# Kernel optimization log

Hardware: AMD Instinct MI355X
Metric: run time of the kernel (lower is better)

The kernel has to match this reference:

```python
import jax, jax.numpy as jnp
import numpy as np

B, T, V, H, OUT = 1024, 128, 89, 256, 1


def setup_inputs() -> dict:
    key = jax.random.key(0)
    ks = jax.random.split(key, 16)
    x = jax.random.normal(ks[0], (B, T, V), dtype=jnp.float32)
    mask = (jax.random.uniform(ks[1], (B, T, V)) < 0.7).astype(jnp.float32)
    deltas = jax.random.uniform(ks[2], (B, T, V), dtype=jnp.float32)
    meanset = jax.random.normal(ks[3], (V,), dtype=jnp.float32)

    def uni(k, shape, fan):
        s = 1.0 / np.sqrt(fan)
        return jax.random.uniform(k, shape, jnp.float32, -s, s)

    # Decay h: Linear(V -> H); Decay x: diag Linear(V -> V)
    W_h = uni(ks[4], (H, V), V)
    b_h = uni(ks[5], (H,), V)
    W_x = uni(ks[6], (V, V), V)
    b_x = uni(ks[7], (V,), V)
    # GRUCell(2V -> H), torch layout: W_ih [3H, 2V], W_hh [3H, H]
    W_ih = uni(ks[8], (3 * H, 2 * V), 2 * V)
    b_ih = uni(ks[9], (3 * H,), 2 * V)
    W_hh = uni(ks[10], (3 * H, H), H)
    b_hh = uni(ks[11], (3 * H,), H)
    # classification head
    W_cls = uni(ks[12], (OUT, H), H)
    b_cls = uni(ks[13], (OUT,), H)
    return {"x": x, "mask": mask, "deltas": deltas, "meanset": meanset,
            "W_h": W_h, "b_h": b_h, "W_x": W_x, "b_x": b_x,
            "W_ih": W_ih, "b_ih": b_ih, "W_hh": W_hh, "b_hh": b_hh,
            "W_cls": W_cls, "b_cls": b_cls}


def reference(x, mask, deltas, meanset, W_h, b_h, W_x, b_x,
              W_ih, b_ih, W_hh, b_hh, W_cls, b_cls):
    Bn, Tn, Vn = x.shape
    Hn = W_h.shape[0]
    # diag Decay: W * eye(V) -> only the diagonal of W_x contributes
    w_x_diag = jnp.diagonal(W_x)

    def step(carry, inp):
        h, last, loss = carry
        x_t, m_t, d_t = inp  # each [B, V]
        gamma_h = jnp.exp(-jax.nn.relu(d_t @ W_h.T + b_h))          # [B, H]
        gamma_x = jnp.exp(-jax.nn.relu(d_t * w_x_diag + b_x))       # [B, V]
        # forward-fill (pandas ffill includes current observation)
        last = jnp.where(m_t > 0, x_t, last)
        h = h * gamma_h
        x_u = gamma_x * last + (1.0 - gamma_x) * meanset
        loss = loss + jnp.sum(jnp.abs(x_t - x_u) * m_t) / (jnp.sum(m_t) + 1e-5)
        x_h = m_t * x_t + (1.0 - m_t) * x_u
        inp_cat = jnp.concatenate([x_h, m_t], axis=1)               # [B, 2V]
        gi = inp_cat @ W_ih.T + b_ih
        gh = h @ W_hh.T + b_hh
        i_r, i_z, i_n = jnp.split(gi, 3, axis=1)
        h_r, h_z, h_n = jnp.split(gh, 3, axis=1)
        r = jax.nn.sigmoid(i_r + h_r)
        z = jax.nn.sigmoid(i_z + h_z)
        n = jnp.tanh(i_n + r * h_n)
        h = (1.0 - z) * n + z * h
        return (h, last, loss), x_h

    init = (jnp.zeros((Bn, Hn), x.dtype), jnp.zeros((Bn, Vn), x.dtype),
            jnp.zeros((), x.dtype))
    xs = (jnp.swapaxes(x, 0, 1), jnp.swapaxes(mask, 0, 1), jnp.swapaxes(deltas, 0, 1))
    (h, _, x_loss), ximp = jax.lax.scan(step, init, xs)
    x_imp = jnp.swapaxes(ximp, 0, 1)                                # [B, T, V]
    # dropout is identity at eval time
    y_out = h @ W_cls.T + b_cls
    y_score = jax.nn.sigmoid(y_out)
    return x_imp, x_loss, y_out, y_score
```

## Files before the change

### kernel.cpp

```cpp
#include <hip/hip_runtime.h>

#define B_  1024
#define T_  128
#define V_  89
#define H_  256
#define NB2 256

typedef __attribute__((ext_vector_type(8))) short bf16x8;
typedef __attribute__((ext_vector_type(4))) float f32x4;
typedef __attribute__((ext_vector_type(4))) unsigned short u16x4;
typedef __attribute__((ext_vector_type(8))) int i32x8;
typedef __attribute__((ext_vector_type(4))) int i32x4;

__device__ __forceinline__ short f2bs(float f){
    unsigned u = __float_as_uint(f);
    unsigned r = (u + 0x7FFFu + ((u>>16)&1u)) >> 16;
    return (short)r;
}
__device__ __forceinline__ float s2f(unsigned short s){
    return __uint_as_float(((unsigned)s) << 16);
}
__device__ __forceinline__ float sig_(float x){ return 1.f/(1.f+__expf(-x)); }
__device__ __forceinline__ float tanh_(float x){ return 2.f/(1.f+__expf(-2.f*x)) - 1.f; }

__global__ __launch_bounds__(256) void k_cvt_fp8(
    const float* __restrict__ src, unsigned char* __restrict__ dst, int n)
{
    int i = blockIdx.x*256 + threadIdx.x;
    if (i*4 >= n) return;
    float f0 = src[i*4+0], f1 = src[i*4+1], f2 = src[i*4+2], f3 = src[i*4+3];
    int w = __builtin_amdgcn_cvt_pk_fp8_f32(f0, f1, 0, false);
    w     = __builtin_amdgcn_cvt_pk_fp8_f32(f2, f3, w, true);
    ((int*)dst)[i] = w;
}

__global__ __launch_bounds__(256) void k_prep_wih8(
    const float* __restrict__ W_ih, const float* __restrict__ b_ih,
    unsigned char* __restrict__ dst)
{
    int i = blockIdx.x*256 + threadIdx.x;
    if (i >= 18432) return;
    int l15 = i & 15, t = i >> 4;
    int g8 = t & 3; t >>= 2;
    int kt = t % 6; t /= 6;
    int g = t % 3, WV = t / 3;
    int n = g*256 + WV*16 + l15;
    float f[8];
    #pragma unroll
    for (int j = 0; j < 8; ++j) {
        int k = kt*32 + g8*8 + j;
        f[j] = (k < 178) ? W_ih[(size_t)n*178 + k] : (k == 178 ? b_ih[n] : 0.f);
    }
    int w0 = __builtin_amdgcn_cvt_pk_fp8_f32(f[0], f[1], 0, false);
    w0     = __builtin_amdgcn_cvt_pk_fp8_f32(f[2], f[3], w0, true);
    int w1 = __builtin_amdgcn_cvt_pk_fp8_f32(f[4], f[5], 0, false);
    w1     = __builtin_amdgcn_cvt_pk_fp8_f32(f[6], f[7], w1, true);
    ((int*)dst)[i*2]   = w0;
    ((int*)dst)[i*2+1] = w1;
}

__global__ __launch_bounds__(256) void k_prep_whp(
    const float* __restrict__ W_h, const float* __restrict__ b_h,
    short* __restrict__ dst)
{
    int i = blockIdx.x*256 + threadIdx.x;
    if (i >= 256*96) return;
    int n = i / 96, k = i - n*96;
    float v = (k < V_) ? W_h[(size_t)n*V_ + k] : (k == V_ ? b_h[n] : 0.f);
    dst[i] = f2bs(v);
}

__global__ __launch_bounds__(512) void k_prep(
    const float* __restrict__ x, const float* __restrict__ mask,
    const float* __restrict__ deltas, const float* __restrict__ meanset,
    const float* __restrict__ W_x, const float* __restrict__ b_x,
    const unsigned char* __restrict__ wihT, const short* __restrict__ whp,
    float* __restrict__ ximp, float* __restrict__ lastst,
    float* __restrict__ numpart, float* __restrict__ denpart,
    unsigned short* __restrict__ gi4, int t0, int TC, int first)
{
    __shared__ unsigned char xl[16*200] __attribute__((aligned(16)));
    __shared__ short dl2[16*104] __attribute__((aligned(16)));
    __shared__ float lossn[4][360], lossd[4][360];
    int tid = threadIdx.x, lane = tid & 63, wv = tid >> 6;
    int l15 = lane & 15, g8 = lane >> 4;
    int blk = blockIdx.x;

    for (int i = tid; i < 16*22; i += 512) {
        int r = i/22, k = 178 + (i - r*22);
        xl[r*200 + k] = (k == 178) ? 0x38 : 0;
    }
    for (int i = tid; i < 16*15; i += 512) {
        int r = i/15, k = 89 + (i - r*15);
        dl2[r*104 + k] = (k == 89) ? (short)0x3F80 : (short)0;
    }
    bool own = tid < 4*V_;
    int r_o = tid / V_, v_o = tid - r_o*V_, b_o = blk*4 + r_o;
    float wxd = 0.f, bx = 0.f, mnv = 0.f, lastv = 0.f;
    if (own) {
        wxd = W_x[v_o*V_ + v_o]; bx = b_x[v_o]; mnv = meanset[v_o];
        lastv = first ? 0.f : lastst[(size_t)b_o*V_ + v_o];
    }
    const long* wT = (const long*)wihT;

    int nph = TC >> 2;
    for (int p = 0; p < nph; ++p) {
        int tg = t0 + p*4;
        __syncthreads();
        if (own) {
            const float* xb = x      + ((size_t)b_o*T_ + tg)*V_ + v_o;
            const float* mb = mask   + ((size_t)b_o*T_ + tg)*V_ + v_o;
            const float* db = deltas + ((size_t)b_o*T_ + tg)*V_ + v_o;
            float xv[4], mv[4], dv[4];
            #pragma unroll
            for (int lt = 0; lt < 4; ++lt) {
                xv[lt] = xb[lt*V_]; mv[lt] = mb[lt*V_]; dv[lt] = db[lt*V_];
            }
            #pragma unroll
            for (int lt = 0; lt < 4; ++lt) {
                float xt = xv[lt], m = mv[lt], d = dv[lt];
                float gx = __expf(-fmaxf(fmaf(d, wxd, bx), 0.f));
                lastv = (m > 0.f) ? xt : lastv;
                float xu = gx*lastv + (1.f-gx)*mnv;
                float xh = m*xt + (1.f-m)*xu;
                ximp[((size_t)b_o*T_ + tg + lt)*V_ + v_o] = xh;
                int mr = r_o*4 + lt;
                int pk = __builtin_amdgcn_cvt_pk_fp8_f32(xh, m, 0, false);
                xl[mr*200 + v_o]      = (unsigned char)(pk & 0xFF);
                xl[mr*200 + V_ + v_o] = (unsigned char)((pk >> 8) & 0xFF);
                dl2[mr*104 + v_o]     = f2bs(d);
                lossn[lt][tid] = fabsf(xt - xu)*m;
                lossd[lt][tid] = m;
            }
        }
        __syncthreads();
        if (tid < 64) {
            int lt = tid >> 4, part = tid & 15;
            float n = 0.f, ds = 0.f;
            for (int j = part; j < 4*V_; j += 16) { n += lossn[lt][j]; ds += lossd[lt][j]; }
            n += __shfl_xor(n, 1); ds += __shfl_xor(ds, 1);
            n += __shfl_xor(n, 2); ds += __shfl_xor(ds, 2);
            n += __shfl_xor(n, 4); ds += __shfl_xor(ds, 4);
            n += __shfl_xor(n, 8); ds += __shfl_xor(ds, 8);
            if (part == 0) {
                numpart[(size_t)(tg+lt)*NB2 + blk] = n;
                denpart[(size_t)(tg+lt)*NB2 + blk] = ds;
            }
        }
        #pragma unroll
        for (int s = 0; s < 2; ++s) {
            int cset = wv + s*8;
            size_t iw = (size_t)cset*1152 + g8*16 + l15;
            f32x4 ar = {0.f,0.f,0.f,0.f}, az = ar, an = ar, ga = ar;
            #pragma unroll
            for (int kt = 0; kt < 6; ++kt) {
                long a = *(const long*)&xl[l15*200 + kt*32 + g8*8];
                ar = __builtin_amdgcn_mfma_f32_16x16x32_fp8_fp8(a, wT[iw +       kt*64], ar, 0,0,0);
                az = __builtin_amdgcn_mfma_f32_16x16x32_fp8_fp8(a, wT[iw + 384 + kt*64], az, 0,0,0);
                an = __builtin_amdgcn_mfma_f32_16x16x32_fp8_fp8(a, wT[iw + 768 + kt*64], an, 0,0,0);
            }
            int cg = cset*16 + l15;
            #pragma unroll
            for (int kt = 0; kt < 3; ++kt) {
                bf16x8 da = *(const bf16x8*)&dl2[l15*104 + kt*32 + g8*8];
                bf16x8 gw = *(const bf16x8*)(whp + (size_t)cg*96 + kt*32 + g8*8);
                ga = __builtin_amdgcn_mfma_f32_16x16x32_bf16(da, gw, ga, 0,0,0);
            }
            #pragma unroll
            for (int rr = 0; rr < 4; ++rr) {
                int ltc = p*4 + rr;
                u16x4 v;
                v[0] = (unsigned short)f2bs(ar[rr]);
                v[1] = (unsigned short)f2bs(az[rr]);
                v[2] = (unsigned short)f2bs(an[rr]);
                v[3] = (unsigned short)f2bs(__expf(-fmaxf(ga[rr], 0.f)));
                ((u16x4*)gi4)[(((size_t)ltc*256 + blk)*4 + g8)*256 + cg] = v;
            }
        }
    }
    if (own) lastst[(size_t)b_o*V_ + v_o] = lastv;
}

__global__ __launch_bounds__(512) void k_recur(
    const unsigned short* __restrict__ gi4, const unsigned char* __restrict__ whh8,
    const float* __restrict__ b_hh, const float* __restrict__ W_cls,
    const float* __restrict__ b_cls,
    float* __restrict__ hstate, float* __restrict__ yout, float* __restrict__ yscore,
    int TC, int first, int last)
{
    __shared__ unsigned char whL[256*256];
    __shared__ unsigned char hlds[2][4*272] __attribute__((aligned(16)));
    __shared__ float yred[4][8];

    int tid = threadIdx.x, lane = tid & 63, wv = tid >> 6;
    int l15 = lane & 15, g8 = lane >> 4;
    int blk = blockIdx.x;
    int c0 = wv*16 + l15, c1 = c0 + 128;

    for (int it = 0; it < 16; ++it) {
        int idx = it*512 + tid;
        int row = idx >> 5, j = idx & 31;
        long v = *(const long*)(whh8 + (size_t)row*256 + j*8);
        *(long*)&whL[row*256 + ((j*8) ^ ((row & 15) << 4))] = v;
    }
    i32x8 wz[2][2], wn[2][2];
    #pragma unroll
    for (int s = 0; s < 2; ++s) {
        int cs16 = (wv + s*8)*16 + l15;
        #pragma unroll
        for (int k2 = 0; k2 < 2; ++k2) {
            wz[s][k2] = *(const i32x8*)(whh8 + (size_t)(256 + cs16)*256 + k2*128 + g8*32);
            wn[s][k2] = *(const i32x8*)(whh8 + (size_t)(512 + cs16)*256 + k2*128 + g8*32);
        }
    }
    float bhr[2], bhz[2], bhn[2];
    #pragma unroll
    for (int s = 0; s < 2; ++s) {
        int cs16 = (wv + s*8)*16 + l15;
        bhr[s] = b_hh[cs16]; bhz[s] = b_hh[256 + cs16]; bhn[s] = b_hh[512 + cs16];
    }

    float h0 = first ? 0.f : hstate[(size_t)(blk*4 + g8)*H_ + c0];
    float h1 = first ? 0.f : hstate[(size_t)(blk*4 + g8)*H_ + c1];

    __syncthreads();

    const u16x4* gp = (const u16x4*)gi4;
#define GIDX(LT,C) ((((size_t)(LT)*256 + blk)*4 + g8)*256 + (C))
    u16x4 gv0 = gp[GIDX(0, c0)], gv1 = gp[GIDX(0, c1)];

    for (int lt = 0; lt < TC; ++lt) {
        int cb = lt & 1;
        float hd0 = h0 * s2f(gv0[3]);
        float hd1 = h1 * s2f(gv1[3]);
        int pk = __builtin_amdgcn_cvt_pk_fp8_f32(hd0, hd1, 0, false);
        hlds[cb][g8*272 + c0] = (unsigned char)(pk & 0xFF);
        hlds[cb][g8*272 + c1] = (unsigned char)((pk >> 8) & 0xFF);
        __syncthreads();
        i32x8 A[2];
        #pragma unroll
        for (int k2 = 0; k2 < 2; ++k2) {
            const unsigned char* ap = &hlds[cb][(l15 >> 2)*272 + k2*128 + g8*32];
            i32x4 lo = *(const i32x4*)(ap);
            i32x4 hi = *(const i32x4*)(ap + 16);
            i32x8 a; a[0]=lo[0]; a[1]=lo[1]; a[2]=lo[2]; a[3]=lo[3];
                     a[4]=hi[0]; a[5]=hi[1]; a[6]=hi[2]; a[7]=hi[3];
            A[k2] = a;
        }
        u16x4 ngv0 = gv0, ngv1 = gv1;
        if (lt + 1 < TC) { ngv0 = gp[GIDX(lt+1, c0)]; ngv1 = gp[GIDX(lt+1, c1)]; }
        int sw = l15 << 4;
        #pragma unroll
        for (int s = 0; s < 2; ++s) {
            const unsigned char* wb = &whL[(size_t)((wv + s*8)*16 + l15)*256];
            f32x4 sr = {bhr[s],bhr[s],bhr[s],bhr[s]};
            f32x4 sz = {bhz[s],bhz[s],bhz[s],bhz[s]};
            f32x4 sn = {bhn[s],bhn[s],bhn[s],bhn[s]};
            #pragma unroll
            for (int k2 = 0; k2 < 2; ++k2) {
                int ob = k2*128 + g8*32;
                i32x4 blo = *(const i32x4*)(wb + ((ob     ) ^ sw));
                i32x4 bhi = *(const i32x4*)(wb + ((ob + 16) ^ sw));
                i32x8 b; b[0]=blo[0]; b[1]=blo[1]; b[2]=blo[2]; b[3]=blo[3];
                         b[4]=bhi[0]; b[5]=bhi[1]; b[6]=bhi[2]; b[7]=bhi[3];
                sr = __builtin_amdgcn_mfma_scale_f32_16x16x128_f8f6f4(A[k2], b,         sr, 0,0, 0,0x7F7F7F7F, 0,0x7F7F7F7F);
                sz = __builtin_amdgcn_mfma_scale_f32_16x16x128_f8f6f4(A[k2], wz[s][k2], sz, 0,0, 0,0x7F7F7F7F, 0,0x7F7F7F7F);
                sn = __builtin_amdgcn_mfma_scale_f32_16x16x128_f8f6f4(A[k2], wn[s][k2], sn, 0,0, 0,0x7F7F7F7F, 0,0x7F7F7F7F);
            }
            if (s == 0) {
                float rg = sig_(s2f(gv0[0]) + sr[0]);
                float zg = sig_(s2f(gv0[1]) + sz[0]);
                float ng = tanh_(s2f(gv0[2]) + rg*sn[0]);
                h0 = (1.f - zg)*ng + zg*hd0;
            } else {
                float rg = sig_(s2f(gv1[0]) + sr[0]);
                float zg = sig_(s2f(gv1[1]) + sz[0]);
                float ng = tanh_(s2f(gv1[2]) + rg*sn[0]);
                h1 = (1.f - zg)*ng + zg*hd1;
            }
        }
        gv0 = ngv0; gv1 = ngv1;
    }
#undef GIDX

    hstate[(size_t)(blk*4 + g8)*H_ + c0] = h0;
    hstate[(size_t)(blk*4 + g8)*H_ + c1] = h1;

    if (last) {
        float pr = h0 * W_cls[c0] + h1 * W_cls[c1];
        pr += __shfl_xor(pr, 1);
        pr += __shfl_xor(pr, 2);
        pr += __shfl_xor(pr, 4);
        pr += __shfl_xor(pr, 8);
        if (l15 == 0) yred[g8][wv] = pr;
        __syncthreads();
        if (tid < 4) {
            float sacc = b_cls[0];
            #pragma unroll
            for (int ww = 0; ww < 8; ++ww) sacc += yred[tid][ww];
            yout[blk*4 + tid]   = sacc;
            yscore[blk*4 + tid] = 1.f/(1.f+__expf(-sacc));
        }
    }
}

__global__ __launch_bounds__(256) void k_loss_t(
    const float* __restrict__ numpart, const float* __restrict__ denpart,
    float* __restrict__ tpart)
{
    int t = blockIdx.x, tid = threadIdx.x;
    float n = numpart[(size_t)t*NB2 + tid];
    float d = denpart[(size_t)t*NB2 + tid];
    for (int off = 32; off; off >>= 1) { n += __shfl_down(n, off); d += __shfl_down(d, off); }
    __shared__ float sn[4], sd[4];
    int lane = tid & 63, wid = tid >> 6;
    if (lane == 0) { sn[wid] = n; sd[wid] = d; }
    __syncthreads();
    if (tid == 0) {
        float nn = sn[0]+sn[1]+sn[2]+sn[3], dd = sd[0]+sd[1]+sd[2]+sd[3];
        tpart[t] = nn / (dd + 1e-5f);
    }
}

__global__ __launch_bounds__(128) void k_loss_final(
    const float* __restrict__ tpart, float* __restrict__ out_loss)
{
    int tid = threadIdx.x;
    float s = tpart[tid];
    for (int off = 32; off; off >>= 1) s += __shfl_down(s, off);
    __shared__ float sp[2];
    if ((tid&63)==0) sp[tid>>6] = s;
    __syncthreads();
    if (tid==0) out_loss[0] = sp[0] + sp[1];
}

static inline size_t al256(size_t x){ return (x + 255) & ~(size_t)255; }

extern "C" void kernel_launch(void* const* d_in, const int* in_sizes, int n_in,
                              void* d_out, int out_size, void* d_ws, size_t ws_size,
                              hipStream_t stream)
{
    const float* x      = (const float*)d_in[0];
    const float* mask   = (const float*)d_in[1];
    const float* deltas = (const float*)d_in[2];
    const float* meanset= (const float*)d_in[3];
    const float* W_h    = (const float*)d_in[4];
    const float* b_h    = (const float*)d_in[5];
    const float* W_x    = (const float*)d_in[6];
    const float* b_x    = (const float*)d_in[7];
    const float* W_ih   = (const float*)d_in[8];
    const float* b_ih   = (const float*)d_in[9];
    const float* W_hh   = (const float*)d_in[10];
    const float* b_hh   = (const float*)d_in[11];
    const float* W_cls  = (const float*)d_in[12];
    const float* b_cls  = (const float*)d_in[13];

    float* out    = (float*)d_out;
    float* ximp   = out;
    float* xloss  = out + (size_t)B_*T_*V_;
    float* yout   = xloss + 1;
    float* yscore = yout + B_;

    size_t off = 0;
    size_t off_whh8 = off; off = al256(off + (size_t)768*256);
    size_t off_wihT = off; off = al256(off + (size_t)768*192);
    size_t off_whp  = off; off = al256(off + (size_t)256*96*2);
    size_t off_last = off; off = al256(off + (size_t)B_*V_*4);
    size_t off_h    = off; off = al256(off + (size_t)B_*H_*4);
    size_t off_np   = off; off = al256(off + (size_t)T_*NB2*4);
    size_t off_dp   = off; off = al256(off + (size_t)T_*NB2*4);
    size_t off_tp   = off; off = al256(off + (size_t)T_*4);
    size_t off_gi4  = off;

    int tcShift = -1;
    for (int s = 7; s >= 2; --s) {
        size_t gib = (size_t)(1 << s) * 256 * 4 * 256 * 8;
        if (off_gi4 + gib <= ws_size) { tcShift = s; break; }
    }
    if (tcShift < 0) return;
    int TC = 1 << tcShift;
    int NC = T_ / TC;

    char* ws = (char*)d_ws;
    unsigned char* whh8 = (unsigned char*)(ws + off_whh8);
    unsigned char* wihT = (unsigned char*)(ws + off_wihT);
    short* whp    = (short*)(ws + off_whp);
    float* lastst = (float*)(ws + off_last);
    float* hstate = (float*)(ws + off_h);
    float* numpart= (float*)(ws + off_np);
    float* denpart= (float*)(ws + off_dp);
    float* tpart  = (float*)(ws + off_tp);
    unsigned short* gi4 = (unsigned short*)(ws + off_gi4);

    hipLaunchKernelGGL(k_cvt_fp8, dim3((768*256/4+255)/256), dim3(256), 0, stream, W_hh, whh8, 768*256);
    hipLaunchKernelGGL(k_prep_wih8, dim3((18432+255)/256), dim3(256), 0, stream, W_ih, b_ih, wihT);
    hipLaunchKernelGGL(k_prep_whp, dim3((256*96+255)/256), dim3(256), 0, stream, W_h, b_h, whp);

    for (int ci = 0; ci < NC; ++ci) {
        int t0 = ci * TC;
        hipLaunchKernelGGL(k_prep, dim3(256), dim3(512), 0, stream,
                           x, mask, deltas, meanset, W_x, b_x, wihT, whp,
                           ximp, lastst, numpart, denpart, gi4, t0, TC, ci==0);
        hipLaunchKernelGGL(k_recur, dim3(256), dim3(512), 0, stream,
                           gi4, whh8, b_hh, W_cls, b_cls,
                           hstate, yout, yscore, TC, ci==0, ci==NC-1);
    }
    hipLaunchKernelGGL(k_loss_t, dim3(T_), dim3(256), 0, stream, numpart, denpart, tpart);
    hipLaunchKernelGGL(k_loss_final, dim3(1), dim3(128), 0, stream, tpart, xloss);
}
```

Before: 269.0 us.

## Split imputation into its own kernel, parallelize gate GEMM over time, widen recurrence blocks

Imputation and the forward-fill scan move into a dedicated kernel with one thread per (batch, variable). It writes an fp8 packed x/mask buffer and per-wave loss partials, so the serial time loop no longer sits inside the gate kernel. The gate projection becomes a separate kernel with a 2D grid over time groups, so all timesteps in a chunk are computed in parallel. The recurrence kernel uses 1024 threads with one hidden column per thread instead of two, and prefetches gates two steps ahead. The cost is an extra global round trip through the fp8 buffer, a serial 128-step loop in the imputation kernel, and higher register pressure in the recurrence.

```diff
diff --git a/kernel.cpp b/kernel.cpp
--- a/kernel.cpp
+++ b/kernel.cpp
@@ -5,6 +5,8 @@
 #define V_  89
 #define H_  256
 #define NB2 256
+#define NBLK1 356
+#define NW1   (NBLK1*4)
 
 typedef __attribute__((ext_vector_type(8))) short bf16x8;
 typedef __attribute__((ext_vector_type(4))) float f32x4;
@@ -70,118 +72,109 @@
     dst[i] = f2bs(v);
 }
 
-__global__ __launch_bounds__(512) void k_prep(
+__global__ __launch_bounds__(256) void k_impute(
     const float* __restrict__ x, const float* __restrict__ mask,
     const float* __restrict__ deltas, const float* __restrict__ meanset,
     const float* __restrict__ W_x, const float* __restrict__ b_x,
+    float* __restrict__ ximp, unsigned char* __restrict__ xm8,
+    float* __restrict__ num_part, float* __restrict__ den_part)
+{
+    int tid = threadIdx.x;
+    int i = blockIdx.x*256 + tid;
+    int b = i / V_, v = i - b*V_;
+    float wxd = W_x[v*V_ + v];
+    float bx  = b_x[v];
+    float mv  = meanset[v];
+    const float* xp = x      + (size_t)b*T_*V_ + v;
+    const float* mp = mask   + (size_t)b*T_*V_ + v;
+    const float* dp = deltas + (size_t)b*T_*V_ + v;
+    float*       op = ximp   + (size_t)b*T_*V_ + v;
+    unsigned char* qp = xm8  + ((size_t)b*T_*V_ + v)*2;
+    float last = 0.f;
+    int lane = tid & 63, wid = tid >> 6;
+    int gw = blockIdx.x*4 + wid;
+    for (int t = 0; t < T_; ++t) {
+        float xt = xp[t*V_], m = mp[t*V_], d = dp[t*V_];
+        float g = __expf(-fmaxf(fmaf(d, wxd, bx), 0.f));
+        last = (m > 0.f) ? xt : last;
+        float xu = g*last + (1.f-g)*mv;
+        float xh = m*xt + (1.f-m)*xu;
+        op[t*V_] = xh;
+        int pk = __builtin_amdgcn_cvt_pk_fp8_f32(xh, m, 0, false);
+        *(unsigned short*)(qp + (size_t)t*V_*2) = (unsigned short)(pk & 0xFFFF);
+        float nv = fabsf(xt - xu)*m;
+        float dv = m;
+        for (int off = 32; off; off >>= 1) {
+            nv += __shfl_down(nv, off);
+            dv += __shfl_down(dv, off);
+        }
+        if (lane == 0) { num_part[t*NW1 + gw] = nv; den_part[t*NW1 + gw] = dv; }
+    }
+}
+
+__global__ __launch_bounds__(512) void k_gates(
+    const unsigned char* __restrict__ xm8, const float* __restrict__ deltas,
     const unsigned char* __restrict__ wihT, const short* __restrict__ whp,
-    float* __restrict__ ximp, float* __restrict__ lastst,
-    float* __restrict__ numpart, float* __restrict__ denpart,
-    unsigned short* __restrict__ gi4, int t0, int TC, int first)
+    unsigned short* __restrict__ gi4, int t0)
 {
     __shared__ unsigned char xl[16*200] __attribute__((aligned(16)));
     __shared__ short dl2[16*104] __attribute__((aligned(16)));
-    __shared__ float lossn[4][360], lossd[4][360];
     int tid = threadIdx.x, lane = tid & 63, wv = tid >> 6;
     int l15 = lane & 15, g8 = lane >> 4;
-    int blk = blockIdx.x;
-
-    for (int i = tid; i < 16*22; i += 512) {
-        int r = i/22, k = 178 + (i - r*22);
+    int bg = blockIdx.x, ph = blockIdx.y;
+    int tg = t0 + ph*4;
+
+    for (int i = tid; i < 16*14; i += 512) {
+        int r = i/14, k = 178 + (i - r*14);
         xl[r*200 + k] = (k == 178) ? 0x38 : 0;
     }
     for (int i = tid; i < 16*15; i += 512) {
         int r = i/15, k = 89 + (i - r*15);
         dl2[r*104 + k] = (k == 89) ? (short)0x3F80 : (short)0;
     }
-    bool own = tid < 4*V_;
-    int r_o = tid / V_, v_o = tid - r_o*V_, b_o = blk*4 + r_o;
-    float wxd = 0.f, bx = 0.f, mnv = 0.f, lastv = 0.f;
-    if (own) {
-        wxd = W_x[v_o*V_ + v_o]; bx = b_x[v_o]; mnv = meanset[v_o];
-        lastv = first ? 0.f : lastst[(size_t)b_o*V_ + v_o];
-    }
+    for (int i = tid; i < 16*V_; i += 512) {
+        int r = i / V_, v = i - r*V_;
+        int b = bg*4 + (r >> 2), t = tg + (r & 3);
+        unsigned short pk = *(const unsigned short*)(xm8 + ((size_t)(b*T_ + t)*V_ + v)*2);
+        xl[r*200 + v]      = (unsigned char)(pk & 0xFF);
+        xl[r*200 + V_ + v] = (unsigned char)(pk >> 8);
+        dl2[r*104 + v]     = f2bs(deltas[((size_t)b*T_ + t)*V_ + v]);
+    }
+    __syncthreads();
     const long* wT = (const long*)wihT;
-
-    int nph = TC >> 2;
-    for (int p = 0; p < nph; ++p) {
-        int tg = t0 + p*4;
-        __syncthreads();
-        if (own) {
-            const float* xb = x      + ((size_t)b_o*T_ + tg)*V_ + v_o;
-            const float* mb = mask   + ((size_t)b_o*T_ + tg)*V_ + v_o;
-            const float* db = deltas + ((size_t)b_o*T_ + tg)*V_ + v_o;
-            float xv[4], mv[4], dv[4];
-            #pragma unroll
-            for (int lt = 0; lt < 4; ++lt) {
-                xv[lt] = xb[lt*V_]; mv[lt] = mb[lt*V_]; dv[lt] = db[lt*V_];
-            }
-            #pragma unroll
-            for (int lt = 0; lt < 4; ++lt) {
-                float xt = xv[lt], m = mv[lt], d = dv[lt];
-                float gx = __expf(-fmaxf(fmaf(d, wxd, bx), 0.f));
-                lastv = (m > 0.f) ? xt : lastv;
-                float xu = gx*lastv + (1.f-gx)*mnv;
-                float xh = m*xt + (1.f-m)*xu;
-                ximp[((size_t)b_o*T_ + tg + lt)*V_ + v_o] = xh;
-                int mr = r_o*4 + lt;
-                int pk = __builtin_amdgcn_cvt_pk_fp8_f32(xh, m, 0, false);
-                xl[mr*200 + v_o]      = (unsigned char)(pk & 0xFF);
-                xl[mr*200 + V_ + v_o] = (unsigned char)((pk >> 8) & 0xFF);
-                dl2[mr*104 + v_o]     = f2bs(d);
-                lossn[lt][tid] = fabsf(xt - xu)*m;
-                lossd[lt][tid] = m;
-            }
-        }
-        __syncthreads();
-        if (tid < 64) {
-            int lt = tid >> 4, part = tid & 15;
-            float n = 0.f, ds = 0.f;
-            for (int j = part; j < 4*V_; j += 16) { n += lossn[lt][j]; ds += lossd[lt][j]; }
-            n += __shfl_xor(n, 1); ds += __shfl_xor(ds, 1);
-            n += __shfl_xor(n, 2); ds += __shfl_xor(ds, 2);
-            n += __shfl_xor(n, 4); ds += __shfl_xor(ds, 4);
-            n += __shfl_xor(n, 8); ds += __shfl_xor(ds, 8);
-            if (part == 0) {
-                numpart[(size_t)(tg+lt)*NB2 + blk] = n;
-                denpart[(size_t)(tg+lt)*NB2 + blk] = ds;
-            }
-        }
-        #pragma unroll
-        for (int s = 0; s < 2; ++s) {
-            int cset = wv + s*8;
-            size_t iw = (size_t)cset*1152 + g8*16 + l15;
-            f32x4 ar = {0.f,0.f,0.f,0.f}, az = ar, an = ar, ga = ar;
-            #pragma unroll
-            for (int kt = 0; kt < 6; ++kt) {
-                long a = *(const long*)&xl[l15*200 + kt*32 + g8*8];
-                ar = __builtin_amdgcn_mfma_f32_16x16x32_fp8_fp8(a, wT[iw +       kt*64], ar, 0,0,0);
-                az = __builtin_amdgcn_mfma_f32_16x16x32_fp8_fp8(a, wT[iw + 384 + kt*64], az, 0,0,0);
-                an = __builtin_amdgcn_mfma_f32_16x16x32_fp8_fp8(a, wT[iw + 768 + kt*64], an, 0,0,0);
-            }
-            int cg = cset*16 + l15;
-            #pragma unroll
-            for (int kt = 0; kt < 3; ++kt) {
-                bf16x8 da = *(const bf16x8*)&dl2[l15*104 + kt*32 + g8*8];
-                bf16x8 gw = *(const bf16x8*)(whp + (size_t)cg*96 + kt*32 + g8*8);
-                ga = __builtin_amdgcn_mfma_f32_16x16x32_bf16(da, gw, ga, 0,0,0);
-            }
-            #pragma unroll
-            for (int rr = 0; rr < 4; ++rr) {
-                int ltc = p*4 + rr;
-                u16x4 v;
-                v[0] = (unsigned short)f2bs(ar[rr]);
-                v[1] = (unsigned short)f2bs(az[rr]);
-                v[2] = (unsigned short)f2bs(an[rr]);
-                v[3] = (unsigned short)f2bs(__expf(-fmaxf(ga[rr], 0.f)));
-                ((u16x4*)gi4)[(((size_t)ltc*256 + blk)*4 + g8)*256 + cg] = v;
-            }
-        }
-    }
-    if (own) lastst[(size_t)b_o*V_ + v_o] = lastv;
-}
-
-__global__ __launch_bounds__(512) void k_recur(
+    #pragma unroll
+    for (int s = 0; s < 2; ++s) {
+        int cset = wv + s*8;
+        size_t iw = (size_t)cset*1152 + g8*16 + l15;
+        f32x4 ar = {0.f,0.f,0.f,0.f}, az = ar, an = ar, ga = ar;
+        #pragma unroll
+        for (int kt = 0; kt < 6; ++kt) {
+            long a = *(const long*)&xl[l15*200 + kt*32 + g8*8];
+            ar = __builtin_amdgcn_mfma_f32_16x16x32_fp8_fp8(a, wT[iw +       kt*64], ar, 0,0,0);
+            az = __builtin_amdgcn_mfma_f32_16x16x32_fp8_fp8(a, wT[iw + 384 + kt*64], az, 0,0,0);
+            an = __builtin_amdgcn_mfma_f32_16x16x32_fp8_fp8(a, wT[iw + 768 + kt*64], an, 0,0,0);
+        }
+        int cg = cset*16 + l15;
+        #pragma unroll
+        for (int kt = 0; kt < 3; ++kt) {
+            bf16x8 da = *(const bf16x8*)&dl2[l15*104 + kt*32 + g8*8];
+            bf16x8 gw = *(const bf16x8*)(whp + (size_t)cg*96 + kt*32 + g8*8);
+            ga = __builtin_amdgcn_mfma_f32_16x16x32_bf16(da, gw, ga, 0,0,0);
+        }
+        #pragma unroll
+        for (int rr = 0; rr < 4; ++rr) {
+            int ltc = ph*4 + rr;
+            u16x4 v;
+            v[0] = (unsigned short)f2bs(ar[rr]);
+            v[1] = (unsigned short)f2bs(az[rr]);
+            v[2] = (unsigned short)f2bs(an[rr]);
+            v[3] = (unsigned short)f2bs(__expf(-fmaxf(ga[rr], 0.f)));
+            ((u16x4*)gi4)[(((size_t)ltc*256 + bg)*4 + g8)*256 + cg] = v;
+        }
+    }
+}
+
+__global__ __launch_bounds__(1024) void k_recur(
     const unsigned short* __restrict__ gi4, const unsigned char* __restrict__ whh8,
     const float* __restrict__ b_hh, const float* __restrict__ W_cls,
     const float* __restrict__ b_cls,
@@ -190,53 +183,53 @@
 {
     __shared__ unsigned char whL[256*256];
     __shared__ unsigned char hlds[2][4*272] __attribute__((aligned(16)));
-    __shared__ float yred[4][8];
-
-    int tid = threadIdx.x, lane = tid & 63, wv = tid >> 6;
+    __shared__ float yred[4][16];
+
+    int tid = threadIdx.x, lane = tid & 63, wv16 = tid >> 6;
     int l15 = lane & 15, g8 = lane >> 4;
     int blk = blockIdx.x;
-    int c0 = wv*16 + l15, c1 = c0 + 128;
-
-    for (int it = 0; it < 16; ++it) {
-        int idx = it*512 + tid;
+    int c = wv16*16 + l15;
+
+    #pragma unroll
+    for (int it = 0; it < 8; ++it) {
+        int idx = it*1024 + tid;
         int row = idx >> 5, j = idx & 31;
         long v = *(const long*)(whh8 + (size_t)row*256 + j*8);
         *(long*)&whL[row*256 + ((j*8) ^ ((row & 15) << 4))] = v;
     }
-    i32x8 wz[2][2], wn[2][2];
-    #pragma unroll
-    for (int s = 0; s < 2; ++s) {
-        int cs16 = (wv + s*8)*16 + l15;
-        #pragma unroll
-        for (int k2 = 0; k2 < 2; ++k2) {
-            wz[s][k2] = *(const i32x8*)(whh8 + (size_t)(256 + cs16)*256 + k2*128 + g8*32);
-            wn[s][k2] = *(const i32x8*)(whh8 + (size_t)(512 + cs16)*256 + k2*128 + g8*32);
-        }
-    }
-    float bhr[2], bhz[2], bhn[2];
-    #pragma unroll
-    for (int s = 0; s < 2; ++s) {
-        int cs16 = (wv + s*8)*16 + l15;
-        bhr[s] = b_hh[cs16]; bhz[s] = b_hh[256 + cs16]; bhn[s] = b_hh[512 + cs16];
-    }
-
-    float h0 = first ? 0.f : hstate[(size_t)(blk*4 + g8)*H_ + c0];
-    float h1 = first ? 0.f : hstate[(size_t)(blk*4 + g8)*H_ + c1];
-
+    i32x8 wz[2], wn[2];
+    #pragma unroll
+    for (int k2 = 0; k2 < 2; ++k2) {
+        wz[k2] = *(const i32x8*)(whh8 + (size_t)(256 + c)*256 + k2*128 + g8*32);
+        wn[k2] = *(const i32x8*)(whh8 + (size_t)(512 + c)*256 + k2*128 + g8*32);
+    }
+    #pragma unroll
+    for (int k2 = 0; k2 < 2; ++k2) {
+        #pragma unroll
+        for (int j = 0; j < 8; ++j) {
+            asm volatile("" : "+v"(wz[k2][j]));
+            asm volatile("" : "+v"(wn[k2][j]));
+        }
+    }
+    float bhr = b_hh[c], bhz = b_hh[256 + c], bhn = b_hh[512 + c];
+    float h = first ? 0.f : hstate[(size_t)(blk*4 + g8)*H_ + c];
     __syncthreads();
 
     const u16x4* gp = (const u16x4*)gi4;
-#define GIDX(LT,C) ((((size_t)(LT)*256 + blk)*4 + g8)*256 + (C))
-    u16x4 gv0 = gp[GIDX(0, c0)], gv1 = gp[GIDX(0, c1)];
+#define GIDX(LT) ((((size_t)(LT)*256 + blk)*4 + g8)*256 + c)
+    u16x4 gv0 = gp[GIDX(0)];
+    u16x4 gv1 = (TC > 1) ? gp[GIDX(1)] : gv0;
+    int sw = l15 << 4;
+    const unsigned char* wb = &whL[(size_t)c*256];
 
     for (int lt = 0; lt < TC; ++lt) {
         int cb = lt & 1;
-        float hd0 = h0 * s2f(gv0[3]);
-        float hd1 = h1 * s2f(gv1[3]);
-        int pk = __builtin_amdgcn_cvt_pk_fp8_f32(hd0, hd1, 0, false);
-        hlds[cb][g8*272 + c0] = (unsigned char)(pk & 0xFF);
-        hlds[cb][g8*272 + c1] = (unsigned char)((pk >> 8) & 0xFF);
+        float hd = h * s2f(gv0[3]);
+        int pk = __builtin_amdgcn_cvt_pk_fp8_f32(hd, hd, 0, false);
+        hlds[cb][g8*272 + c] = (unsigned char)(pk & 0xFF);
         __syncthreads();
+        u16x4 gv2 = gv1;
+        if (lt + 2 < TC) gv2 = gp[GIDX(lt + 2)];
         i32x8 A[2];
         #pragma unroll
         for (int k2 = 0; k2 < 2; ++k2) {
@@ -247,57 +240,42 @@
                      a[4]=hi[0]; a[5]=hi[1]; a[6]=hi[2]; a[7]=hi[3];
             A[k2] = a;
         }
-        u16x4 ngv0 = gv0, ngv1 = gv1;
-        if (lt + 1 < TC) { ngv0 = gp[GIDX(lt+1, c0)]; ngv1 = gp[GIDX(lt+1, c1)]; }
-        int sw = l15 << 4;
-        #pragma unroll
-        for (int s = 0; s < 2; ++s) {
-            const unsigned char* wb = &whL[(size_t)((wv + s*8)*16 + l15)*256];
-            f32x4 sr = {bhr[s],bhr[s],bhr[s],bhr[s]};
-            f32x4 sz = {bhz[s],bhz[s],bhz[s],bhz[s]};
-            f32x4 sn = {bhn[s],bhn[s],bhn[s],bhn[s]};
-            #pragma unroll
-            for (int k2 = 0; k2 < 2; ++k2) {
-                int ob = k2*128 + g8*32;
-                i32x4 blo = *(const i32x4*)(wb + ((ob     ) ^ sw));
-                i32x4 bhi = *(const i32x4*)(wb + ((ob + 16) ^ sw));
-                i32x8 b; b[0]=blo[0]; b[1]=blo[1]; b[2]=blo[2]; b[3]=blo[3];
-                         b[4]=bhi[0]; b[5]=bhi[1]; b[6]=bhi[2]; b[7]=bhi[3];
-                sr = __builtin_amdgcn_mfma_scale_f32_16x16x128_f8f6f4(A[k2], b,         sr, 0,0, 0,0x7F7F7F7F, 0,0x7F7F7F7F);
-                sz = __builtin_amdgcn_mfma_scale_f32_16x16x128_f8f6f4(A[k2], wz[s][k2], sz, 0,0, 0,0x7F7F7F7F, 0,0x7F7F7F7F);
-                sn = __builtin_amdgcn_mfma_scale_f32_16x16x128_f8f6f4(A[k2], wn[s][k2], sn, 0,0, 0,0x7F7F7F7F, 0,0x7F7F7F7F);
-            }
-            if (s == 0) {
-                float rg = sig_(s2f(gv0[0]) + sr[0]);
-                float zg = sig_(s2f(gv0[1]) + sz[0]);
-                float ng = tanh_(s2f(gv0[2]) + rg*sn[0]);
-                h0 = (1.f - zg)*ng + zg*hd0;
-            } else {
-                float rg = sig_(s2f(gv1[0]) + sr[0]);
-                float zg = sig_(s2f(gv1[1]) + sz[0]);
-                float ng = tanh_(s2f(gv1[2]) + rg*sn[0]);
-                h1 = (1.f - zg)*ng + zg*hd1;
-            }
-        }
-        gv0 = ngv0; gv1 = ngv1;
+        f32x4 sr = {bhr,bhr,bhr,bhr};
+        f32x4 sz = {bhz,bhz,bhz,bhz};
+        f32x4 sn = {bhn,bhn,bhn,bhn};
+        #pragma unroll
+        for (int k2 = 0; k2 < 2; ++k2) {
+            int ob = k2*128 + g8*32;
+            i32x4 blo = *(const i32x4*)(wb + ((ob     ) ^ sw));
+            i32x4 bhi = *(const i32x4*)(wb + ((ob + 16) ^ sw));
+            i32x8 b; b[0]=blo[0]; b[1]=blo[1]; b[2]=blo[2]; b[3]=blo[3];
+                     b[4]=bhi[0]; b[5]=bhi[1]; b[6]=bhi[2]; b[7]=bhi[3];
+            sr = __builtin_amdgcn_mfma_scale_f32_16x16x128_f8f6f4(A[k2], b,      sr, 0,0, 0,0x7F7F7F7F, 0,0x7F7F7F7F);
+            sz = __builtin_amdgcn_mfma_scale_f32_16x16x128_f8f6f4(A[k2], wz[k2], sz, 0,0, 0,0x7F7F7F7F, 0,0x7F7F7F7F);
+            sn = __builtin_amdgcn_mfma_scale_f32_16x16x128_f8f6f4(A[k2], wn[k2], sn, 0,0, 0,0x7F7F7F7F, 0,0x7F7F7F7F);
+        }
+        float rg = sig_(s2f(gv0[0]) + sr[0]);
+        float zg = sig_(s2f(gv0[1]) + sz[0]);
+        float ng = tanh_(s2f(gv0[2]) + rg*sn[0]);
+        h = (1.f - zg)*ng + zg*hd;
+        gv0 = gv1; gv1 = gv2;
     }
 #undef GIDX
 
-    hstate[(size_t)(blk*4 + g8)*H_ + c0] = h0;
-    hstate[(size_t)(blk*4 + g8)*H_ + c1] = h1;
+    hstate[(size_t)(blk*4 + g8)*H_ + c] = h;
 
     if (last) {
-        float pr = h0 * W_cls[c0] + h1 * W_cls[c1];
+        float pr = h * W_cls[c];
         pr += __shfl_xor(pr, 1);
         pr += __shfl_xor(pr, 2);
         pr += __shfl_xor(pr, 4);
         pr += __shfl_xor(pr, 8);
-        if (l15 == 0) yred[g8][wv] = pr;
+        if (l15 == 0) yred[g8][wv16] = pr;
         __syncthreads();
         if (tid < 4) {
             float sacc = b_cls[0];
             #pragma unroll
-            for (int ww = 0; ww < 8; ++ww) sacc += yred[tid][ww];
+            for (int ww = 0; ww < 16; ++ww) sacc += yred[tid][ww];
             yout[blk*4 + tid]   = sacc;
             yscore[blk*4 + tid] = 1.f/(1.f+__expf(-sacc));
         }
@@ -305,20 +283,20 @@
 }
 
 __global__ __launch_bounds__(256) void k_loss_t(
-    const float* __restrict__ numpart, const float* __restrict__ denpart,
+    const float* __restrict__ num_part, const float* __restrict__ den_part,
     float* __restrict__ tpart)
 {
     int t = blockIdx.x, tid = threadIdx.x;
-    float n = numpart[(size_t)t*NB2 + tid];
-    float d = denpart[(size_t)t*NB2 + tid];
-    for (int off = 32; off; off >>= 1) { n += __shfl_down(n, off); d += __shfl_down(d, off); }
+    float num = 0.f, den = 0.f;
+    for (int j = tid; j < NW1; j += 256) { num += num_part[t*NW1+j]; den += den_part[t*NW1+j]; }
+    for (int off = 32; off; off >>= 1) { num += __shfl_down(num, off); den += __shfl_down(den, off); }
     __shared__ float sn[4], sd[4];
     int lane = tid & 63, wid = tid >> 6;
-    if (lane == 0) { sn[wid] = n; sd[wid] = d; }
+    if (lane == 0) { sn[wid] = num; sd[wid] = den; }
     __syncthreads();
     if (tid == 0) {
-        float nn = sn[0]+sn[1]+sn[2]+sn[3], dd = sd[0]+sd[1]+sd[2]+sd[3];
-        tpart[t] = nn / (dd + 1e-5f);
+        float n = sn[0]+sn[1]+sn[2]+sn[3], d = sd[0]+sd[1]+sd[2]+sd[3];
+        tpart[t] = n / (d + 1e-5f);
     }
 }
 
@@ -365,10 +343,10 @@
     size_t off_whh8 = off; off = al256(off + (size_t)768*256);
     size_t off_wihT = off; off = al256(off + (size_t)768*192);
     size_t off_whp  = off; off = al256(off + (size_t)256*96*2);
-    size_t off_last = off; off = al256(off + (size_t)B_*V_*4);
+    size_t off_xm8  = off; off = al256(off + (size_t)B_*T_*V_*2);
     size_t off_h    = off; off = al256(off + (size_t)B_*H_*4);
-    size_t off_np   = off; off = al256(off + (size_t)T_*NB2*4);
-    size_t off_dp   = off; off = al256(off + (size_t)T_*NB2*4);
+    size_t off_np   = off; off = al256(off + (size_t)T_*NW1*4);
+    size_t off_dp   = off; off = al256(off + (size_t)T_*NW1*4);
     size_t off_tp   = off; off = al256(off + (size_t)T_*4);
     size_t off_gi4  = off;
 
@@ -385,7 +363,7 @@
     unsigned char* whh8 = (unsigned char*)(ws + off_whh8);
     unsigned char* wihT = (unsigned char*)(ws + off_wihT);
     short* whp    = (short*)(ws + off_whp);
-    float* lastst = (float*)(ws + off_last);
+    unsigned char* xm8 = (unsigned char*)(ws + off_xm8);
     float* hstate = (float*)(ws + off_h);
     float* numpart= (float*)(ws + off_np);
     float* denpart= (float*)(ws + off_dp);
@@ -395,16 +373,17 @@
     hipLaunchKernelGGL(k_cvt_fp8, dim3((768*256/4+255)/256), dim3(256), 0, stream, W_hh, whh8, 768*256);
     hipLaunchKernelGGL(k_prep_wih8, dim3((18432+255)/256), dim3(256), 0, stream, W_ih, b_ih, wihT);
     hipLaunchKernelGGL(k_prep_whp, dim3((256*96+255)/256), dim3(256), 0, stream, W_h, b_h, whp);
+    hipLaunchKernelGGL(k_impute, dim3(NBLK1), dim3(256), 0, stream,
+                       x, mask, deltas, meanset, W_x, b_x, ximp, xm8, numpart, denpart);
+    hipLaunchKernelGGL(k_loss_t, dim3(T_), dim3(256), 0, stream, numpart, denpart, tpart);
+    hipLaunchKernelGGL(k_loss_final, dim3(1), dim3(128), 0, stream, tpart, xloss);
 
     for (int ci = 0; ci < NC; ++ci) {
         int t0 = ci * TC;
-        hipLaunchKernelGGL(k_prep, dim3(256), dim3(512), 0, stream,
-                           x, mask, deltas, meanset, W_x, b_x, wihT, whp,
-                           ximp, lastst, numpart, denpart, gi4, t0, TC, ci==0);
-        hipLaunchKernelGGL(k_recur, dim3(256), dim3(512), 0, stream,
+        hipLaunchKernelGGL(k_gates, dim3(256, TC/4), dim3(512), 0, stream,
+                           xm8, deltas, wihT, whp, gi4, t0);
+        hipLaunchKernelGGL(k_recur, dim3(256), dim3(1024), 0, stream,
                            gi4, whh8, b_hh, W_cls, b_cls,
                            hstate, yout, yscore, TC, ci==0, ci==NC-1);
     }
-    hipLaunchKernelGGL(k_loss_t, dim3(T_), dim3(256), 0, stream, numpart, denpart, tpart);
-    hipLaunchKernelGGL(k_loss_final, dim3(1), dim3(128), 0, stream, tpart, xloss);
-}
+}
```

Measured after the change: 398.4 us. +48.1%, slower.

## Split GRU recurrence across 16 waves with one hidden column per thread

Applied to the files above, without the earlier changes.

The recurrent kernel now launches 1024 threads per block, so each wave owns one 16-column slice instead of two. This halves the serial MFMA chain and gate math per wave on each timestep. It also swaps __syncthreads for an explicit lgkmcnt wait plus barrier, prefetches gate inputs two steps ahead, and raises wave priority around the MFMA block. In exchange, more waves join each per-step barrier and register pressure rises, since the 1024-thread launch bound limits VGPRs per thread.

```diff
diff --git a/kernel.cpp b/kernel.cpp
--- a/kernel.cpp
+++ b/kernel.cpp
@@ -22,6 +22,10 @@
 }
 __device__ __forceinline__ float sig_(float x){ return 1.f/(1.f+__expf(-x)); }
 __device__ __forceinline__ float tanh_(float x){ return 2.f/(1.f+__expf(-2.f*x)) - 1.f; }
+__device__ __forceinline__ void bar_lgkm(){
+    asm volatile("s_waitcnt lgkmcnt(0)" ::: "memory");
+    __builtin_amdgcn_s_barrier();
+}
 
 __global__ __launch_bounds__(256) void k_cvt_fp8(
     const float* __restrict__ src, unsigned char* __restrict__ dst, int n)
@@ -181,7 +185,7 @@
     if (own) lastst[(size_t)b_o*V_ + v_o] = lastv;
 }
 
-__global__ __launch_bounds__(512) void k_recur(
+__global__ __launch_bounds__(1024) void k_recur(
     const unsigned short* __restrict__ gi4, const unsigned char* __restrict__ whh8,
     const float* __restrict__ b_hh, const float* __restrict__ W_cls,
     const float* __restrict__ b_cls,
@@ -190,53 +194,53 @@
 {
     __shared__ unsigned char whL[256*256];
     __shared__ unsigned char hlds[2][4*272] __attribute__((aligned(16)));
-    __shared__ float yred[4][8];
-
-    int tid = threadIdx.x, lane = tid & 63, wv = tid >> 6;
+    __shared__ float yred[4][16];
+
+    int tid = threadIdx.x, lane = tid & 63, wv16 = tid >> 6;
     int l15 = lane & 15, g8 = lane >> 4;
     int blk = blockIdx.x;
-    int c0 = wv*16 + l15, c1 = c0 + 128;
-
-    for (int it = 0; it < 16; ++it) {
-        int idx = it*512 + tid;
+    int c = wv16*16 + l15;
+
+    #pragma unroll
+    for (int it = 0; it < 8; ++it) {
+        int idx = it*1024 + tid;
         int row = idx >> 5, j = idx & 31;
         long v = *(const long*)(whh8 + (size_t)row*256 + j*8);
         *(long*)&whL[row*256 + ((j*8) ^ ((row & 15) << 4))] = v;
     }
-    i32x8 wz[2][2], wn[2][2];
+    i32x8 wz[2], wn[2];
     #pragma unroll
-    for (int s = 0; s < 2; ++s) {
-        int cs16 = (wv + s*8)*16 + l15;
+    for (int k2 = 0; k2 < 2; ++k2) {
+        wz[k2] = *(const i32x8*)(whh8 + (size_t)(256 + c)*256 + k2*128 + g8*32);
+        wn[k2] = *(const i32x8*)(whh8 + (size_t)(512 + c)*256 + k2*128 + g8*32);
+    }
+    #pragma unroll
+    for (int k2 = 0; k2 < 2; ++k2) {
         #pragma unroll
-        for (int k2 = 0; k2 < 2; ++k2) {
-            wz[s][k2] = *(const i32x8*)(whh8 + (size_t)(256 + cs16)*256 + k2*128 + g8*32);
-            wn[s][k2] = *(const i32x8*)(whh8 + (size_t)(512 + cs16)*256 + k2*128 + g8*32);
-        }
-    }
-    float bhr[2], bhz[2], bhn[2];
-    #pragma unroll
-    for (int s = 0; s < 2; ++s) {
-        int cs16 = (wv + s*8)*16 + l15;
-        bhr[s] = b_hh[cs16]; bhz[s] = b_hh[256 + cs16]; bhn[s] = b_hh[512 + cs16];
-    }
-
-    float h0 = first ? 0.f : hstate[(size_t)(blk*4 + g8)*H_ + c0];
-    float h1 = first ? 0.f : hstate[(size_t)(blk*4 + g8)*H_ + c1];
-
+        for (int j = 0; j < 8; ++j) {
+            asm volatile("" : "+v"(wz[k2][j]));
+            asm volatile("" : "+v"(wn[k2][j]));
+        }
+    }
+    float bhr = b_hh[c], bhz = b_hh[256 + c], bhn = b_hh[512 + c];
+    float h = first ? 0.f : hstate[(size_t)(blk*4 + g8)*H_ + c];
     __syncthreads();
 
     const u16x4* gp = (const u16x4*)gi4;
-#define GIDX(LT,C) ((((size_t)(LT)*256 + blk)*4 + g8)*256 + (C))
-    u16x4 gv0 = gp[GIDX(0, c0)], gv1 = gp[GIDX(0, c1)];
+#define GIDX(LT) ((((size_t)(LT)*256 + blk)*4 + g8)*256 + c)
+    u16x4 gv0 = gp[GIDX(0)];
+    u16x4 gv1 = (TC > 1) ? gp[GIDX(1)] : gv0;
+    int sw = l15 << 4;
+    const unsigned char* wb = &whL[(size_t)c*256];
 
     for (int lt = 0; lt < TC; ++lt) {
         int cb = lt & 1;
-        float hd0 = h0 * s2f(gv0[3]);
-        float hd1 = h1 * s2f(gv1[3]);
-        int pk = __builtin_amdgcn_cvt_pk_fp8_f32(hd0, hd1, 0, false);
-        hlds[cb][g8*272 + c0] = (unsigned char)(pk & 0xFF);
-        hlds[cb][g8*272 + c1] = (unsigned char)((pk >> 8) & 0xFF);
-        __syncthreads();
+        float hd = h * s2f(gv0[3]);
+        int pk = __builtin_amdgcn_cvt_pk_fp8_f32(hd, hd, 0, false);
+        hlds[cb][g8*272 + c] = (unsigned char)(pk & 0xFF);
+        bar_lgkm();
+        u16x4 gv2 = gv1;
+        if (lt + 2 < TC) gv2 = gp[GIDX(lt + 2)];
         i32x8 A[2];
         #pragma unroll
         for (int k2 = 0; k2 < 2; ++k2) {
@@ -247,57 +251,44 @@
                      a[4]=hi[0]; a[5]=hi[1]; a[6]=hi[2]; a[7]=hi[3];
             A[k2] = a;
         }
-        u16x4 ngv0 = gv0, ngv1 = gv1;
-        if (lt + 1 < TC) { ngv0 = gp[GIDX(lt+1, c0)]; ngv1 = gp[GIDX(lt+1, c1)]; }
-        int sw = l15 << 4;
+        f32x4 sr = {bhr,bhr,bhr,bhr};
+        f32x4 sz = {bhz,bhz,bhz,bhz};
+        f32x4 sn = {bhn,bhn,bhn,bhn};
+        __builtin_amdgcn_s_setprio(1);
         #pragma unroll
-        for (int s = 0; s < 2; ++s) {
-            const unsigned char* wb = &whL[(size_t)((wv + s*8)*16 + l15)*256];
-            f32x4 sr = {bhr[s],bhr[s],bhr[s],bhr[s]};
-            f32x4 sz = {bhz[s],bhz[s],bhz[s],bhz[s]};
-            f32x4 sn = {bhn[s],bhn[s],bhn[s],bhn[s]};
-            #pragma unroll
-            for (int k2 = 0; k2 < 2; ++k2) {
-                int ob = k2*128 + g8*32;
-                i32x4 blo = *(const i32x4*)(wb + ((ob     ) ^ sw));
-                i32x4 bhi = *(const i32x4*)(wb + ((ob + 16) ^ sw));
-                i32x8 b; b[0]=blo[0]; b[1]=blo[1]; b[2]=blo[2]; b[3]=blo[3];
-                         b[4]=bhi[0]; b[5]=bhi[1]; b[6]=bhi[2]; b[7]=bhi[3];
-                sr = __builtin_amdgcn_mfma_scale_f32_16x16x128_f8f6f4(A[k2], b,         sr, 0,0, 0,0x7F7F7F7F, 0,0x7F7F7F7F);
-                sz = __builtin_amdgcn_mfma_scale_f32_16x16x128_f8f6f4(A[k2], wz[s][k2], sz, 0,0, 0,0x7F7F7F7F, 0,0x7F7F7F7F);
-                sn = __builtin_amdgcn_mfma_scale_f32_16x16x128_f8f6f4(A[k2], wn[s][k2], sn, 0,0, 0,0x7F7F7F7F, 0,0x7F7F7F7F);
-            }
-            if (s == 0) {
-                float rg = sig_(s2f(gv0[0]) + sr[0]);
-                float zg = sig_(s2f(gv0[1]) + sz[0]);
-                float ng = tanh_(s2f(gv0[2]) + rg*sn[0]);
-                h0 = (1.f - zg)*ng + zg*hd0;
-            } else {
-                float rg = sig_(s2f(gv1[0]) + sr[0]);
-                float zg = sig_(s2f(gv1[1]) + sz[0]);
-                float ng = tanh_(s2f(gv1[2]) + rg*sn[0]);
-                h1 = (1.f - zg)*ng + zg*hd1;
-            }
-        }
-        gv0 = ngv0; gv1 = ngv1;
+        for (int k2 = 0; k2 < 2; ++k2) {
+            int ob = k2*128 + g8*32;
+            i32x4 blo = *(const i32x4*)(wb + ((ob     ) ^ sw));
+            i32x4 bhi = *(const i32x4*)(wb + ((ob + 16) ^ sw));
+            i32x8 b; b[0]=blo[0]; b[1]=blo[1]; b[2]=blo[2]; b[3]=blo[3];
+                     b[4]=bhi[0]; b[5]=bhi[1]; b[6]=bhi[2]; b[7]=bhi[3];
+            sr = __builtin_amdgcn_mfma_scale_f32_16x16x128_f8f6f4(A[k2], b,      sr, 0,0, 0,0x7F7F7F7F, 0,0x7F7F7F7F);
+            sz = __builtin_amdgcn_mfma_scale_f32_16x16x128_f8f6f4(A[k2], wz[k2], sz, 0,0, 0,0x7F7F7F7F, 0,0x7F7F7F7F);
+            sn = __builtin_amdgcn_mfma_scale_f32_16x16x128_f8f6f4(A[k2], wn[k2], sn, 0,0, 0,0x7F7F7F7F, 0,0x7F7F7F7F);
+        }
+        __builtin_amdgcn_s_setprio(0);
+        float rg = sig_(s2f(gv0[0]) + sr[0]);
+        float zg = sig_(s2f(gv0[1]) + sz[0]);
+        float ng = tanh_(s2f(gv0[2]) + rg*sn[0]);
+        h = (1.f - zg)*ng + zg*hd;
+        gv0 = gv1; gv1 = gv2;
     }
 #undef GIDX
 
-    hstate[(size_t)(blk*4 + g8)*H_ + c0] = h0;
-    hstate[(size_t)(blk*4 + g8)*H_ + c1] = h1;
+    hstate[(size_t)(blk*4 + g8)*H_ + c] = h;
 
     if (last) {
-        float pr = h0 * W_cls[c0] + h1 * W_cls[c1];
+        float pr = h * W_cls[c];
         pr += __shfl_xor(pr, 1);
         pr += __shfl_xor(pr, 2);
         pr += __shfl_xor(pr, 4);
         pr += __shfl_xor(pr, 8);
-        if (l15 == 0) yred[g8][wv] = pr;
+        if (l15 == 0) yred[g8][wv16] = pr;
         __syncthreads();
         if (tid < 4) {
             float sacc = b_cls[0];
             #pragma unroll
-            for (int ww = 0; ww < 8; ++ww) sacc += yred[tid][ww];
+            for (int ww = 0; ww < 16; ++ww) sacc += yred[tid][ww];
             yout[blk*4 + tid]   = sacc;
             yscore[blk*4 + tid] = 1.f/(1.f+__expf(-sacc));
         }
@@ -401,7 +392,7 @@
         hipLaunchKernelGGL(k_prep, dim3(256), dim3(512), 0, stream,
                            x, mask, deltas, meanset, W_x, b_x, wihT, whp,
                            ximp, lastst, numpart, denpart, gi4, t0, TC, ci==0);
-        hipLaunchKernelGGL(k_recur, dim3(256), dim3(512), 0, stream,
+        hipLaunchKernelGGL(k_recur, dim3(256), dim3(1024), 0, stream,
                            gi4, whh8, b_hh, W_cls, b_cls,
                            hstate, yout, yscore, TC, ci==0, ci==NC-1);
     }
```

Measured after the change: 273.8 us. Within noise of the previous version (+1.8%).
